# Performance work log

Measured on AMD Instinct MI355X. Metric: run time of the kernel, lower is better.

Reference implementation:

```python
import jax, jax.numpy as jnp
import numpy as np

N = 50000          # nodes
E = 800000         # directed edges (before self-loops)
F_IN = 256
HIDS = 32
HEADS = 8
N_CLASSES = 40
NEG_SLOPE = 0.2    # PyG GATConv default leaky_relu slope


def setup_inputs() -> dict:
    key = jax.random.key(0)
    ks = jax.random.split(key, 10)
    x = jax.random.normal(ks[0], (N, F_IN), dtype=jnp.float32)
    edge_index = jax.random.randint(ks[1], (2, E), 0, N, dtype=jnp.int32)
    # conv1: F_IN -> HIDS per head, HEADS heads, concat=True
    W1 = jax.random.normal(ks[2], (F_IN, HEADS * HIDS), dtype=jnp.float32) * (1.0 / np.sqrt(F_IN))
    a1_src = jax.random.normal(ks[3], (HEADS, HIDS), dtype=jnp.float32) * 0.1
    a1_dst = jax.random.normal(ks[4], (HEADS, HIDS), dtype=jnp.float32) * 0.1
    b1 = jnp.zeros((HEADS * HIDS,), dtype=jnp.float32)
    # conv2: HEADS*HIDS -> N_CLASSES, 1 head, concat=False
    W2 = jax.random.normal(ks[5], (HEADS * HIDS, N_CLASSES), dtype=jnp.float32) * (1.0 / np.sqrt(HEADS * HIDS))
    a2_src = jax.random.normal(ks[6], (1, N_CLASSES), dtype=jnp.float32) * 0.1
    a2_dst = jax.random.normal(ks[7], (1, N_CLASSES), dtype=jnp.float32) * 0.1
    b2 = jnp.zeros((N_CLASSES,), dtype=jnp.float32)
    return {"x": x, "edge_index": edge_index, "W1": W1, "a1_src": a1_src,
            "a1_dst": a1_dst, "b1": b1, "W2": W2, "a2_src": a2_src,
            "a2_dst": a2_dst, "b2": b2}


def _gat_conv(x, src, dst, W, a_src, a_dst, bias, heads, concat):
    n = x.shape[0]
    c = W.shape[1] // heads
    xw = (x @ W).reshape(n, heads, c)                       # [N,H,C]
    alpha_s = jnp.einsum('nhc,hc->nh', xw, a_src)           # [N,H]
    alpha_d = jnp.einsum('nhc,hc->nh', xw, a_dst)
    e = alpha_s[src] + alpha_d[dst]                         # [Etot,H]
    e = jnp.where(e >= 0, e, NEG_SLOPE * e)                 # leaky_relu
    # segment softmax over incoming edges of each destination node
    m = jax.ops.segment_max(e, dst, num_segments=n)         # [N,H]
    ex = jnp.exp(e - m[dst])
    denom = jax.ops.segment_sum(ex, dst, num_segments=n)    # [N,H]
    alpha = ex / denom[dst]                                 # [Etot,H]
    out = jax.ops.segment_sum(alpha[:, :, None] * xw[src], dst, num_segments=n)  # [N,H,C]
    if concat:
        out = out.reshape(n, heads * c)
    else:
        out = out.mean(axis=1)
    return out + bias


def reference(x, edge_index, W1, a1_src, a1_dst, b1, W2, a2_src, a2_dst, b2):
    n = x.shape[0]
    # add self-loops (PyG GATConv default)
    loop = jnp.arange(n, dtype=edge_index.dtype)
    src = jnp.concatenate([edge_index[0], loop])
    dst = jnp.concatenate([edge_index[1], loop])
    # dropout(p=0.6) layers are identity in eval mode
    h = _gat_conv(x, src, dst, W1, a1_src, a1_dst, b1, HEADS, True)
    h = jax.nn.elu(h)
    out = _gat_conv(h, src, dst, W2, a2_src, a2_dst, b2, 1, False)
    return out
```

## Files before the change

### kernel.cpp

```cpp
#include <hip/hip_runtime.h>
#include <hip/hip_bf16.h>

#define NNODES 50000
#define NPAD   50048
#define NEDGES 800000
#define ETOT   (NEDGES + NNODES)
#define FIN    256
#define HIDS   32
#define HEADS  8
#define NCLS   40
#define NEG    0.2f

#define SCAN_B 256
#define NSCB   ((NNODES + SCAN_B - 1) / SCAN_B)

typedef __attribute__((ext_vector_type(8))) short bf16x8;
typedef __attribute__((ext_vector_type(4))) float f32x4;

__device__ __forceinline__ ushort f2bf(float f) {
  unsigned u = __float_as_uint(f);
  unsigned r = (u + 0x7fffu + ((u >> 16) & 1u)) >> 16;
  return (ushort)r;
}
__device__ __forceinline__ float bf2f(ushort u) {
  return __uint_as_float(((unsigned)u) << 16);
}

__global__ __launch_bounds__(256) void prep_k(
    const float* __restrict__ W1, const float* __restrict__ W2,
    const float* __restrict__ a1src, const float* __restrict__ a1dst,
    const float* __restrict__ a2src, const float* __restrict__ a2dst,
    ushort* __restrict__ w1t, ushort* __restrict__ w2t,
    int* __restrict__ cnt, ushort* __restrict__ hb) {
  int b = blockIdx.x, t = threadIdx.x;
  if (b < 256) {
    int k = b, n = t;
    w1t[(size_t)n * 256 + k] = f2bf(W1[(size_t)k * 256 + n]);
  } else if (b < 272) {
    int j = b - 256, k = t;
    const float* av = (j < 8) ? (a1src + j * 32) : (a1dst + (j - 8) * 32);
    int nb = (j < 8) ? j * 32 : (j - 8) * 32;
    float s = 0.f;
#pragma unroll
    for (int c = 0; c < 32; ++c) s += W1[(size_t)k * 256 + nb + c] * av[c];
    w1t[(size_t)(256 + j) * 256 + k] = f2bf(s);
  } else if (b < 320) {
    w1t[(size_t)b * 256 + t] = 0;
  } else if (b < 384) {
    int n = b - 320, k = t;
    ushort v;
    if (n < NCLS) {
      v = f2bf(W2[(size_t)k * NCLS + n]);
    } else if (n == 40) {
      float s = 0.f;
#pragma unroll
      for (int c = 0; c < NCLS; ++c) s += W2[(size_t)k * NCLS + c] * a2src[c];
      v = f2bf(s);
    } else if (n == 41) {
      float s = 0.f;
#pragma unroll
      for (int c = 0; c < NCLS; ++c) s += W2[(size_t)k * NCLS + c] * a2dst[c];
      v = f2bf(s);
    } else {
      v = 0;
    }
    w2t[(size_t)n * 256 + k] = v;
  } else if (b < 580) {
    int i = (b - 384) * 256 + t;
    if (i < NNODES) cnt[i] = 0;
  } else {
    int r = NNODES + (b - 580);
    hb[(size_t)r * 256 + t] = 0;
  }
}

__global__ __launch_bounds__(256) void gemm1_mfma(
    const float* __restrict__ x, const ushort* __restrict__ w1t,
    ushort* __restrict__ xw1b, float* __restrict__ a1s, float* __restrict__ a1d) {
  __shared__ ushort As[64 * 40];
  __shared__ ushort Bs[320 * 40];
  const int tid = threadIdx.x;
  const int m0 = blockIdx.x * 64;
  const int w = tid >> 6, l = tid & 63, lr = l & 15, lq = l >> 4;
  f32x4 acc[4][5];
#pragma unroll
  for (int i = 0; i < 4; ++i)
#pragma unroll
    for (int j = 0; j < 5; ++j) acc[i][j] = (f32x4)0.f;

  for (int k0 = 0; k0 < 256; k0 += 32) {
    {
      int row = tid >> 2, kg = (tid & 3) * 8;
      int gr = m0 + row;
      bf16x8 av;
      if (gr < NNODES) {
        const float4* xp = (const float4*)(x + (size_t)gr * 256 + k0 + kg);
        float4 p0 = xp[0], p1 = xp[1];
        av[0] = (short)f2bf(p0.x); av[1] = (short)f2bf(p0.y);
        av[2] = (short)f2bf(p0.z); av[3] = (short)f2bf(p0.w);
        av[4] = (short)f2bf(p1.x); av[5] = (short)f2bf(p1.y);
        av[6] = (short)f2bf(p1.z); av[7] = (short)f2bf(p1.w);
      } else {
        av = (bf16x8)0;
      }
      *(bf16x8*)&As[row * 40 + kg] = av;
    }
#pragma unroll
    for (int p = 0; p < 5; ++p) {
      int idx = tid + p * 256;
      int n = idx >> 2, kg = (idx & 3) * 8;
      *(bf16x8*)&Bs[n * 40 + kg] = *(const bf16x8*)(w1t + (size_t)n * 256 + k0 + kg);
    }
    __syncthreads();
    bf16x8 af[4], bfr[5];
#pragma unroll
    for (int mt = 0; mt < 4; ++mt)
      af[mt] = *(const bf16x8*)&As[(mt * 16 + lr) * 40 + lq * 8];
#pragma unroll
    for (int nt = 0; nt < 5; ++nt) {
      int tile = nt * 4 + w;
      bfr[nt] = *(const bf16x8*)&Bs[(tile * 16 + lr) * 40 + lq * 8];
    }
#pragma unroll
    for (int mt = 0; mt < 4; ++mt)
#pragma unroll
      for (int nt = 0; nt < 5; ++nt)
        acc[mt][nt] = __builtin_amdgcn_mfma_f32_16x16x32_bf16(af[mt], bfr[nt], acc[mt][nt], 0, 0, 0);
    __syncthreads();
  }
#pragma unroll
  for (int mt = 0; mt < 4; ++mt)
#pragma unroll
    for (int nt = 0; nt < 5; ++nt) {
      int tile = nt * 4 + w;
      if (tile < 16) {
        int colc = tile * 16 + lr;
#pragma unroll
        for (int r = 0; r < 4; ++r) {
          int row = m0 + mt * 16 + lq * 4 + r;
          xw1b[(size_t)row * 256 + colc] = f2bf(acc[mt][nt][r]);
        }
      } else if (tile == 16) {
#pragma unroll
        for (int r = 0; r < 4; ++r) {
          int row = m0 + mt * 16 + lq * 4 + r;
          if (row < NNODES) {
            if (lr < 8) a1s[(size_t)row * 8 + lr] = acc[mt][nt][r];
            else        a1d[(size_t)row * 8 + lr - 8] = acc[mt][nt][r];
          }
        }
      }
    }
}

__global__ __launch_bounds__(256) void gemm2_mfma(
    const ushort* __restrict__ hb, const ushort* __restrict__ w2t,
    ushort* __restrict__ xw2b, float* __restrict__ a2s, float* __restrict__ a2d) {
  const int tid = threadIdx.x;
  const int w = tid >> 6, l = tid & 63, lr = l & 15, lq = l >> 4;
  const int row0 = blockIdx.x * 64 + w * 16;
  f32x4 acc[3];
#pragma unroll
  for (int i = 0; i < 3; ++i) acc[i] = (f32x4)0.f;
#pragma unroll
  for (int ks = 0; ks < 8; ++ks) {
    int k0 = ks * 32;
    bf16x8 af = *(const bf16x8*)(hb + (size_t)(row0 + lr) * 256 + k0 + lq * 8);
#pragma unroll
    for (int nt = 0; nt < 3; ++nt) {
      bf16x8 bfr = *(const bf16x8*)(w2t + (size_t)(nt * 16 + lr) * 256 + k0 + lq * 8);
      acc[nt] = __builtin_amdgcn_mfma_f32_16x16x32_bf16(af, bfr, acc[nt], 0, 0, 0);
    }
  }
#pragma unroll
  for (int nt = 0; nt < 3; ++nt) {
    int colc = nt * 16 + lr;
#pragma unroll
    for (int r = 0; r < 4; ++r) {
      int row = row0 + lq * 4 + r;
      if (colc < NCLS)      xw2b[(size_t)row * 40 + colc] = f2bf(acc[nt][r]);
      else if (colc == 40)  a2s[row] = acc[nt][r];
      else if (colc == 41)  a2d[row] = acc[nt][r];
    }
  }
}

__global__ __launch_bounds__(256) void hist_k(const int* __restrict__ dstA, int* __restrict__ cnt) {
  int e = blockIdx.x * 256 + threadIdx.x;
  if (e >= ETOT) return;
  int d = (e < NEDGES) ? dstA[e] : (e - NEDGES);
  atomicAdd(&cnt[d], 1);
}

__global__ __launch_bounds__(SCAN_B) void scan1_k(const int* __restrict__ deg,
                                                  int* __restrict__ row_ptr,
                                                  int* __restrict__ bsum) {
  __shared__ int sm[SCAN_B];
  int b = blockIdx.x, t = threadIdx.x;
  int idx = b * SCAN_B + t;
  int v = (idx < NNODES) ? deg[idx] : 0;
  sm[t] = v;
  __syncthreads();
#pragma unroll
  for (int off = 1; off < SCAN_B; off <<= 1) {
    int u = (t >= off) ? sm[t - off] : 0;
    __syncthreads();
    sm[t] += u;
    __syncthreads();
  }
  if (idx < NNODES) row_ptr[idx + 1] = sm[t];
  if (t == SCAN_B - 1) bsum[b] = sm[t];
}

__global__ __launch_bounds__(256) void scan2_k(int* __restrict__ bsum) {
  __shared__ int sm[256];
  int t = threadIdx.x;
  sm[t] = (t < NSCB) ? bsum[t] : 0;
  __syncthreads();
#pragma unroll
  for (int off = 1; off < 256; off <<= 1) {
    int u = (t >= off) ? sm[t - off] : 0;
    __syncthreads();
    sm[t] += u;
    __syncthreads();
  }
  if (t < NSCB) bsum[t] = (t > 0) ? sm[t - 1] : 0;
}

__global__ __launch_bounds__(SCAN_B) void scan3_k(const int* __restrict__ bsum,
                                                  int* __restrict__ row_ptr) {
  int b = blockIdx.x, t = threadIdx.x;
  int idx = b * SCAN_B + t;
  if (idx < NNODES) row_ptr[idx + 1] += bsum[b];
  if (b == 0 && t == 0) row_ptr[0] = 0;
}

__global__ __launch_bounds__(256) void scatter_k(const int* __restrict__ srcA, const int* __restrict__ dstA,
                                                 const int* __restrict__ row_ptr, int* __restrict__ cnt,
                                                 int* __restrict__ col) {
  int e = blockIdx.x * 256 + threadIdx.x;
  if (e >= ETOT) return;
  int s, d;
  if (e < NEDGES) { s = srcA[e]; d = dstA[e]; }
  else { s = d = e - NEDGES; }
  int old = atomicSub(&cnt[d], 1);
  col[row_ptr[d] + old - 1] = s;
}

__global__ __launch_bounds__(256) void agg1_k(
    const ushort* __restrict__ xw1b, const float* __restrict__ a1s, const float* __restrict__ a1d,
    const int* __restrict__ row_ptr, const int* __restrict__ col,
    const float* __restrict__ b1, ushort* __restrict__ hb) {
  __shared__ float4 ps[2][64];
  __shared__ float pd[2][64];
  const int tid = threadIdx.x;
  const int wave = tid >> 6, lane = tid & 63;
  const int nl = wave >> 1, sub = wave & 1;
  const int node = blockIdx.x * 2 + nl;
  const int hh = lane >> 3;
  int beg = row_ptr[node], end = row_ptr[node + 1];
  int half = (end - beg + 1) >> 1;
  int i = beg + sub * half;
  int lim = sub ? end : (beg + half);
  float ad = a1d[(size_t)node * 8 + hh];
  float denom = 0.f, ax = 0.f, ay = 0.f, az = 0.f, aw = 0.f;
  for (; i + 4 <= lim; i += 4) {
    int s0 = col[i], s1 = col[i + 1], s2 = col[i + 2], s3 = col[i + 3];
    float e0 = a1s[(size_t)s0 * 8 + hh] + ad;
    float e1 = a1s[(size_t)s1 * 8 + hh] + ad;
    float e2 = a1s[(size_t)s2 * 8 + hh] + ad;
    float e3 = a1s[(size_t)s3 * 8 + hh] + ad;
    ushort4 u0 = *(const ushort4*)(xw1b + (size_t)s0 * 256 + lane * 4);
    ushort4 u1 = *(const ushort4*)(xw1b + (size_t)s1 * 256 + lane * 4);
    ushort4 u2 = *(const ushort4*)(xw1b + (size_t)s2 * 256 + lane * 4);
    ushort4 u3 = *(const ushort4*)(xw1b + (size_t)s3 * 256 + lane * 4);
    float w0 = __expf(fmaxf(e0, 0.f) + NEG * fminf(e0, 0.f));
    float w1 = __expf(fmaxf(e1, 0.f) + NEG * fminf(e1, 0.f));
    float w2 = __expf(fmaxf(e2, 0.f) + NEG * fminf(e2, 0.f));
    float w3 = __expf(fmaxf(e3, 0.f) + NEG * fminf(e3, 0.f));
    denom += (w0 + w1) + (w2 + w3);
    ax += w0 * bf2f(u0.x) + w1 * bf2f(u1.x) + w2 * bf2f(u2.x) + w3 * bf2f(u3.x);
    ay += w0 * bf2f(u0.y) + w1 * bf2f(u1.y) + w2 * bf2f(u2.y) + w3 * bf2f(u3.y);
    az += w0 * bf2f(u0.z) + w1 * bf2f(u1.z) + w2 * bf2f(u2.z) + w3 * bf2f(u3.z);
    aw += w0 * bf2f(u0.w) + w1 * bf2f(u1.w) + w2 * bf2f(u2.w) + w3 * bf2f(u3.w);
  }
  for (; i < lim; ++i) {
    int s = col[i];
    float e = a1s[(size_t)s * 8 + hh] + ad;
    float w = __expf(fmaxf(e, 0.f) + NEG * fminf(e, 0.f));
    ushort4 u = *(const ushort4*)(xw1b + (size_t)s * 256 + lane * 4);
    denom += w;
    ax += w * bf2f(u.x); ay += w * bf2f(u.y); az += w * bf2f(u.z); aw += w * bf2f(u.w);
  }
  if (sub) {
    ps[nl][lane] = make_float4(ax, ay, az, aw);
    pd[nl][lane] = denom;
  }
  __syncthreads();
  if (!sub) {
    float4 o = ps[nl][lane];
    ax += o.x; ay += o.y; az += o.z; aw += o.w;
    denom += pd[nl][lane];
    float inv = 1.f / denom;
    float4 bv = *reinterpret_cast<const float4*>(b1 + lane * 4);
    float ox = ax * inv + bv.x;
    float oy = ay * inv + bv.y;
    float oz = az * inv + bv.z;
    float ow = aw * inv + bv.w;
    ox = (ox > 0.f) ? ox : expm1f(ox);
    oy = (oy > 0.f) ? oy : expm1f(oy);
    oz = (oz > 0.f) ? oz : expm1f(oz);
    ow = (ow > 0.f) ? ow : expm1f(ow);
    ushort4 ho;
    ho.x = f2bf(ox); ho.y = f2bf(oy); ho.z = f2bf(oz); ho.w = f2bf(ow);
    *(ushort4*)(hb + (size_t)node * 256 + lane * 4) = ho;
  }
}

__global__ __launch_bounds__(256) void agg2_k(
    const ushort* __restrict__ xw2b, const float* __restrict__ a2s, const float* __restrict__ a2d,
    const int* __restrict__ row_ptr, const int* __restrict__ col,
    const float* __restrict__ b2, float* __restrict__ out) {
  __shared__ float ps[2][40];
  __shared__ float pd[2];
  const int tid = threadIdx.x;
  const int wave = tid >> 6, lane = tid & 63;
  const int nl = wave >> 1, sub = wave & 1;
  const int node = blockIdx.x * 2 + nl;
  int beg = row_ptr[node], end = row_ptr[node + 1];
  int half = (end - beg + 1) >> 1;
  int i = beg + sub * half;
  int lim = sub ? end : (beg + half);
  float ad = a2d[node];
  float denom = 0.f, acc = 0.f;
  for (; i + 4 <= lim; i += 4) {
    int s0 = col[i], s1 = col[i + 1], s2 = col[i + 2], s3 = col[i + 3];
    float e0 = a2s[s0] + ad;
    float e1 = a2s[s1] + ad;
    float e2 = a2s[s2] + ad;
    float e3 = a2s[s3] + ad;
    float w0 = __expf(fmaxf(e0, 0.f) + NEG * fminf(e0, 0.f));
    float w1 = __expf(fmaxf(e1, 0.f) + NEG * fminf(e1, 0.f));
    float w2 = __expf(fmaxf(e2, 0.f) + NEG * fminf(e2, 0.f));
    float w3 = __expf(fmaxf(e3, 0.f) + NEG * fminf(e3, 0.f));
    float x0 = 0.f, x1 = 0.f, x2 = 0.f, x3 = 0.f;
    if (lane < NCLS) {
      x0 = bf2f(xw2b[(size_t)s0 * 40 + lane]);
      x1 = bf2f(xw2b[(size_t)s1 * 40 + lane]);
      x2 = bf2f(xw2b[(size_t)s2 * 40 + lane]);
      x3 = bf2f(xw2b[(size_t)s3 * 40 + lane]);
    }
    denom += (w0 + w1) + (w2 + w3);
    acc += w0 * x0 + w1 * x1 + w2 * x2 + w3 * x3;
  }
  for (; i < lim; ++i) {
    int s = col[i];
    float e = a2s[s] + ad;
    float w = __expf(fmaxf(e, 0.f) + NEG * fminf(e, 0.f));
    denom += w;
    if (lane < NCLS) acc += w * bf2f(xw2b[(size_t)s * 40 + lane]);
  }
  if (sub) {
    if (lane < NCLS) ps[nl][lane] = acc;
    if (lane == 0) pd[nl] = denom;
  }
  __syncthreads();
  if (!sub) {
    denom += pd[nl];
    if (lane < NCLS) {
      acc += ps[nl][lane];
      out[(size_t)node * 40 + lane] = acc / denom + b2[lane];
    }
  }
}

extern "C" void kernel_launch(void* const* d_in, const int* in_sizes, int n_in,
                              void* d_out, int out_size, void* d_ws, size_t ws_size,
                              hipStream_t stream) {
  const float* x     = (const float*)d_in[0];
  const int*   ei    = (const int*)d_in[1];
  const float* W1    = (const float*)d_in[2];
  const float* a1src = (const float*)d_in[3];
  const float* a1dst = (const float*)d_in[4];
  const float* b1    = (const float*)d_in[5];
  const float* W2    = (const float*)d_in[6];
  const float* a2src = (const float*)d_in[7];
  const float* a2dst = (const float*)d_in[8];
  const float* b2    = (const float*)d_in[9];
  float* out = (float*)d_out;

  const int* srcA = ei;
  const int* dstA = ei + NEDGES;

  ushort* w1t  = (ushort*)d_ws;
  ushort* w2t  = w1t + (size_t)320 * 256;
  ushort* xw1b = w2t + (size_t)64 * 256;
  ushort* hb   = xw1b + (size_t)NPAD * 256;
  ushort* xw2b = hb + (size_t)NPAD * 256;
  float* a1s   = (float*)(xw2b + (size_t)NPAD * 40);
  float* a1d   = a1s + (size_t)NNODES * 8;
  float* a2s   = a1d + (size_t)NNODES * 8;
  float* a2d   = a2s + NPAD;
  int* row_ptr = (int*)(a2d + NPAD);
  int* cnt     = row_ptr + (NNODES + 1);
  int* col     = cnt + NNODES;
  int* bsum    = col + ETOT;

  prep_k<<<628, 256, 0, stream>>>(W1, W2, a1src, a1dst, a2src, a2dst, w1t, w2t, cnt, hb);

  gemm1_mfma<<<NPAD / 64, 256, 0, stream>>>(x, w1t, xw1b, a1s, a1d);

  hist_k<<<(ETOT + 255) / 256, 256, 0, stream>>>(dstA, cnt);
  scan1_k<<<NSCB, SCAN_B, 0, stream>>>(cnt, row_ptr, bsum);
  scan2_k<<<1, 256, 0, stream>>>(bsum);
  scan3_k<<<NSCB, SCAN_B, 0, stream>>>(bsum, row_ptr);
  scatter_k<<<(ETOT + 255) / 256, 256, 0, stream>>>(srcA, dstA, row_ptr, cnt, col);

  agg1_k<<<NNODES / 2, 256, 0, stream>>>(xw1b, a1s, a1d, row_ptr, col, b1, hb);

  gemm2_mfma<<<NPAD / 64, 256, 0, stream>>>(hb, w2t, xw2b, a2s, a2d);

  agg2_k<<<NNODES / 2, 256, 0, stream>>>(xw2b, a2s, a2d, row_ptr, col, b2, out);
}
```

Baseline: 266.1 us.

## Store layer-1 features head-sliced and aggregate one head per block

```diff
diff --git a/kernel.cpp b/kernel.cpp
--- a/kernel.cpp
+++ b/kernel.cpp
@@ -76,7 +76,7 @@
 
 __global__ __launch_bounds__(256) void gemm1_mfma(
     const float* __restrict__ x, const ushort* __restrict__ w1t,
-    ushort* __restrict__ xw1b, float* __restrict__ a1s, float* __restrict__ a1d) {
+    ushort* __restrict__ xw1s, float* __restrict__ a1sx, float* __restrict__ a1dx) {
   __shared__ ushort As[64 * 40];
   __shared__ ushort Bs[320 * 40];
   const int tid = threadIdx.x;
@@ -135,19 +135,18 @@
       int tile = nt * 4 + w;
       if (tile < 16) {
         int colc = tile * 16 + lr;
+        int s = colc >> 5, c = colc & 31;
 #pragma unroll
         for (int r = 0; r < 4; ++r) {
           int row = m0 + mt * 16 + lq * 4 + r;
-          xw1b[(size_t)row * 256 + colc] = f2bf(acc[mt][nt][r]);
+          xw1s[((size_t)s * NPAD + row) * 32 + c] = f2bf(acc[mt][nt][r]);
         }
       } else if (tile == 16) {
 #pragma unroll
         for (int r = 0; r < 4; ++r) {
           int row = m0 + mt * 16 + lq * 4 + r;
-          if (row < NNODES) {
-            if (lr < 8) a1s[(size_t)row * 8 + lr] = acc[mt][nt][r];
-            else        a1d[(size_t)row * 8 + lr - 8] = acc[mt][nt][r];
-          }
+          if (lr < 8) a1sx[(size_t)lr * NPAD + row] = acc[mt][nt][r];
+          else        a1dx[(size_t)(lr - 8) * NPAD + row] = acc[mt][nt][r];
         }
       }
     }
@@ -248,72 +247,63 @@
 }
 
 __global__ __launch_bounds__(256) void agg1_k(
-    const ushort* __restrict__ xw1b, const float* __restrict__ a1s, const float* __restrict__ a1d,
+    const ushort* __restrict__ xw1s, const float* __restrict__ a1sx, const float* __restrict__ a1dx,
     const int* __restrict__ row_ptr, const int* __restrict__ col,
     const float* __restrict__ b1, ushort* __restrict__ hb) {
-  __shared__ float4 ps[2][64];
-  __shared__ float pd[2][64];
+  const int b = blockIdx.x;
+  const int s = b & 7;
   const int tid = threadIdx.x;
   const int wave = tid >> 6, lane = tid & 63;
-  const int nl = wave >> 1, sub = wave & 1;
-  const int node = blockIdx.x * 2 + nl;
-  const int hh = lane >> 3;
-  int beg = row_ptr[node], end = row_ptr[node + 1];
-  int half = (end - beg + 1) >> 1;
-  int i = beg + sub * half;
-  int lim = sub ? end : (beg + half);
-  float ad = a1d[(size_t)node * 8 + hh];
-  float denom = 0.f, ax = 0.f, ay = 0.f, az = 0.f, aw = 0.f;
-  for (; i + 4 <= lim; i += 4) {
-    int s0 = col[i], s1 = col[i + 1], s2 = col[i + 2], s3 = col[i + 3];
-    float e0 = a1s[(size_t)s0 * 8 + hh] + ad;
-    float e1 = a1s[(size_t)s1 * 8 + hh] + ad;
-    float e2 = a1s[(size_t)s2 * 8 + hh] + ad;
-    float e3 = a1s[(size_t)s3 * 8 + hh] + ad;
-    ushort4 u0 = *(const ushort4*)(xw1b + (size_t)s0 * 256 + lane * 4);
-    ushort4 u1 = *(const ushort4*)(xw1b + (size_t)s1 * 256 + lane * 4);
-    ushort4 u2 = *(const ushort4*)(xw1b + (size_t)s2 * 256 + lane * 4);
-    ushort4 u3 = *(const ushort4*)(xw1b + (size_t)s3 * 256 + lane * 4);
-    float w0 = __expf(fmaxf(e0, 0.f) + NEG * fminf(e0, 0.f));
-    float w1 = __expf(fmaxf(e1, 0.f) + NEG * fminf(e1, 0.f));
-    float w2 = __expf(fmaxf(e2, 0.f) + NEG * fminf(e2, 0.f));
-    float w3 = __expf(fmaxf(e3, 0.f) + NEG * fminf(e3, 0.f));
-    denom += (w0 + w1) + (w2 + w3);
-    ax += w0 * bf2f(u0.x) + w1 * bf2f(u1.x) + w2 * bf2f(u2.x) + w3 * bf2f(u3.x);
-    ay += w0 * bf2f(u0.y) + w1 * bf2f(u1.y) + w2 * bf2f(u2.y) + w3 * bf2f(u3.y);
-    az += w0 * bf2f(u0.z) + w1 * bf2f(u1.z) + w2 * bf2f(u2.z) + w3 * bf2f(u3.z);
-    aw += w0 * bf2f(u0.w) + w1 * bf2f(u1.w) + w2 * bf2f(u2.w) + w3 * bf2f(u3.w);
-  }
-  for (; i < lim; ++i) {
-    int s = col[i];
-    float e = a1s[(size_t)s * 8 + hh] + ad;
+  const int node = (b >> 3) * 4 + wave;
+  const int g = lane >> 3, cl = lane & 7;
+  const int beg = row_ptr[node], end = row_ptr[node + 1];
+  const float ad = a1dx[(size_t)s * NPAD + node];
+  const ushort* xs = xw1s + (size_t)s * NPAD * 32;
+  const float* as = a1sx + (size_t)s * NPAD;
+  float d = 0.f, a0 = 0.f, a1 = 0.f, a2 = 0.f, a3 = 0.f;
+  int i = beg;
+  for (; i + 8 <= end; i += 8) {
+    int src = col[i + g];
+    float e = as[src] + ad;
     float w = __expf(fmaxf(e, 0.f) + NEG * fminf(e, 0.f));
-    ushort4 u = *(const ushort4*)(xw1b + (size_t)s * 256 + lane * 4);
-    denom += w;
-    ax += w * bf2f(u.x); ay += w * bf2f(u.y); az += w * bf2f(u.z); aw += w * bf2f(u.w);
-  }
-  if (sub) {
-    ps[nl][lane] = make_float4(ax, ay, az, aw);
-    pd[nl][lane] = denom;
-  }
-  __syncthreads();
-  if (!sub) {
-    float4 o = ps[nl][lane];
-    ax += o.x; ay += o.y; az += o.z; aw += o.w;
-    denom += pd[nl][lane];
-    float inv = 1.f / denom;
-    float4 bv = *reinterpret_cast<const float4*>(b1 + lane * 4);
-    float ox = ax * inv + bv.x;
-    float oy = ay * inv + bv.y;
-    float oz = az * inv + bv.z;
-    float ow = aw * inv + bv.w;
-    ox = (ox > 0.f) ? ox : expm1f(ox);
-    oy = (oy > 0.f) ? oy : expm1f(oy);
-    oz = (oz > 0.f) ? oz : expm1f(oz);
-    ow = (ow > 0.f) ? ow : expm1f(ow);
+    ushort4 u = *(const ushort4*)(xs + (size_t)src * 32 + cl * 4);
+    d += w;
+    a0 += w * bf2f(u.x); a1 += w * bf2f(u.y);
+    a2 += w * bf2f(u.z); a3 += w * bf2f(u.w);
+  }
+  if (i < end) {
+    int idx = i + g;
+    bool v = idx < end;
+    int src = col[v ? idx : beg];
+    float e = as[src] + ad;
+    float w = v ? __expf(fmaxf(e, 0.f) + NEG * fminf(e, 0.f)) : 0.f;
+    ushort4 u = *(const ushort4*)(xs + (size_t)src * 32 + cl * 4);
+    d += w;
+    a0 += w * bf2f(u.x); a1 += w * bf2f(u.y);
+    a2 += w * bf2f(u.z); a3 += w * bf2f(u.w);
+  }
+#pragma unroll
+  for (int off = 8; off < 64; off <<= 1) {
+    d  += __shfl_xor(d, off);
+    a0 += __shfl_xor(a0, off);
+    a1 += __shfl_xor(a1, off);
+    a2 += __shfl_xor(a2, off);
+    a3 += __shfl_xor(a3, off);
+  }
+  if (g == 0) {
+    float inv = 1.f / d;
+    const float4 bv = *reinterpret_cast<const float4*>(b1 + s * 32 + cl * 4);
+    float o0 = a0 * inv + bv.x;
+    float o1 = a1 * inv + bv.y;
+    float o2 = a2 * inv + bv.z;
+    float o3 = a3 * inv + bv.w;
+    o0 = (o0 > 0.f) ? o0 : expm1f(o0);
+    o1 = (o1 > 0.f) ? o1 : expm1f(o1);
+    o2 = (o2 > 0.f) ? o2 : expm1f(o2);
+    o3 = (o3 > 0.f) ? o3 : expm1f(o3);
     ushort4 ho;
-    ho.x = f2bf(ox); ho.y = f2bf(oy); ho.z = f2bf(oz); ho.w = f2bf(ow);
-    *(ushort4*)(hb + (size_t)node * 256 + lane * 4) = ho;
+    ho.x = f2bf(o0); ho.y = f2bf(o1); ho.z = f2bf(o2); ho.w = f2bf(o3);
+    *(ushort4*)(hb + (size_t)node * 256 + s * 32 + cl * 4) = ho;
   }
 }
 
@@ -394,12 +384,12 @@
 
   ushort* w1t  = (ushort*)d_ws;
   ushort* w2t  = w1t + (size_t)320 * 256;
-  ushort* xw1b = w2t + (size_t)64 * 256;
-  ushort* hb   = xw1b + (size_t)NPAD * 256;
+  ushort* xw1s = w2t + (size_t)64 * 256;
+  ushort* hb   = xw1s + (size_t)NPAD * 256;
   ushort* xw2b = hb + (size_t)NPAD * 256;
-  float* a1s   = (float*)(xw2b + (size_t)NPAD * 40);
-  float* a1d   = a1s + (size_t)NNODES * 8;
-  float* a2s   = a1d + (size_t)NNODES * 8;
+  float* a1sx  = (float*)(xw2b + (size_t)NPAD * 40);
+  float* a1dx  = a1sx + (size_t)8 * NPAD;
+  float* a2s   = a1dx + (size_t)8 * NPAD;
   float* a2d   = a2s + NPAD;
   int* row_ptr = (int*)(a2d + NPAD);
   int* cnt     = row_ptr + (NNODES + 1);
@@ -408,7 +398,7 @@
 
   prep_k<<<628, 256, 0, stream>>>(W1, W2, a1src, a1dst, a2src, a2dst, w1t, w2t, cnt, hb);
 
-  gemm1_mfma<<<NPAD / 64, 256, 0, stream>>>(x, w1t, xw1b, a1s, a1d);
+  gemm1_mfma<<<NPAD / 64, 256, 0, stream>>>(x, w1t, xw1s, a1sx, a1dx);
 
   hist_k<<<(ETOT + 255) / 256, 256, 0, stream>>>(dstA, cnt);
   scan1_k<<<NSCB, SCAN_B, 0, stream>>>(cnt, row_ptr, bsum);
@@ -416,7 +406,7 @@
   scan3_k<<<NSCB, SCAN_B, 0, stream>>>(bsum, row_ptr);
   scatter_k<<<(ETOT + 255) / 256, 256, 0, stream>>>(srcA, dstA, row_ptr, cnt, col);
 
-  agg1_k<<<NNODES / 2, 256, 0, stream>>>(xw1b, a1s, a1d, row_ptr, col, b1, hb);
+  agg1_k<<<8 * (NNODES / 4), 256, 0, stream>>>(xw1s, a1sx, a1dx, row_ptr, col, b1, hb);
 
   gemm2_mfma<<<NPAD / 64, 256, 0, stream>>>(hb, w2t, xw2b, a2s, a2d);
 
```

After: 360.5 us. 1.35x slower.
